# Optimization experiments

Measured on AMD Instinct MI355X. Metric: run time of the kernel, lower is better.

Reference implementation:

```python
import jax, jax.numpy as jnp
import numpy as np

B, N, C = 4, 3136, 64
IMG_H = IMG_W = 56
HEADS = 1
TOPK = 8
HID = 4 * C  # mlp_ratio=4.0


def _ln(x, g, b, eps=1e-5):
    m = x.mean(-1, keepdims=True)
    v = ((x - m) ** 2).mean(-1, keepdims=True)
    return (x - m) * jax.lax.rsqrt(v + eps) * g + b


def _conv(x, w, b, pad, groups):
    y = jax.lax.conv_general_dilated(
        x, w, (1, 1), [(pad, pad), (pad, pad)],
        dimension_numbers=('NCHW', 'OIHW', 'NCHW'), feature_group_count=groups)
    return y + b[None, :, None, None]


def setup_inputs() -> dict:
    key = jax.random.key(0)
    ks = jax.random.split(key, 10)
    def rn(k, shp, scale=0.02):
        return jax.random.normal(k, shp, jnp.float32) * scale
    return {
        'x': jax.random.normal(ks[0], (B, N, C), jnp.float32),
        'norm1_g': jnp.ones((C,), jnp.float32), 'norm1_b': jnp.zeros((C,), jnp.float32),
        'wq': rn(ks[1], (C, C)), 'bq': jnp.zeros((C,), jnp.float32),
        'wkv': rn(ks[2], (C, 2 * C)), 'bkv': jnp.zeros((2 * C,), jnp.float32),
        'wproj': rn(ks[3], (C, C)), 'bproj': jnp.zeros((C,), jnp.float32),
        'local_w': rn(ks[4], (C, C // HEADS, 3, 3), 0.05), 'local_b': jnp.zeros((C,), jnp.float32),
        'norm2_g': jnp.ones((C,), jnp.float32), 'norm2_b': jnp.zeros((C,), jnp.float32),
        'w3': rn(ks[5], (HID, 1, 3, 3), 0.05), 'b3': jnp.zeros((HID,), jnp.float32),
        'w5': rn(ks[6], (HID, 1, 5, 5), 0.05), 'b5': jnp.zeros((HID,), jnp.float32),
        'w1': rn(ks[7], (C, 2 * HID, 1, 1), 0.05), 'b1': jnp.zeros((C,), jnp.float32),
        'H': IMG_H, 'W': IMG_W,
    }


def reference(x, norm1_g, norm1_b, wq, bq, wkv, bkv, wproj, bproj,
              local_w, local_b, norm2_g, norm2_b, w3, b3, w5, b5, w1, b1, H, W):
    Bb, Nn, Cc = x.shape
    d = Cc // HEADS
    scale = d ** -0.5
    # --- DynamicSparseAttention (global branch) ---
    xn = _ln(x, norm1_g, norm1_b)
    q = (xn @ wq + bq).reshape(Bb, Nn, HEADS, d).transpose(0, 2, 1, 3)       # bhnd
    kv = (xn @ wkv + bkv).reshape(Bb, Nn, 2, HEADS, d)
    k = kv[:, :, 0].transpose(0, 2, 1, 3)
    v = kv[:, :, 1].transpose(0, 2, 1, 3)
    attn = jnp.einsum('bhnd,bhmd->bhnm', q, k) * scale                        # [B,h,N,N]
    kth = jax.lax.top_k(attn, TOPK)[0][..., -1:]                              # k-th largest per row
    mask = (attn >= kth).astype(attn.dtype)                                   # top-k scatter mask
    p = jax.nn.softmax(attn * mask, axis=-1)                                  # zeros kept (as in torch ref)
    g = jnp.einsum('bhnm,bhmd->bhnd', p, v).transpose(0, 2, 1, 3).reshape(Bb, Nn, Cc)
    g = g @ wproj + bproj
    # --- local conv attention branch ---
    x_img = x.transpose(0, 2, 1).reshape(Bb, Cc, H, W)
    loc = _conv(x_img, local_w, local_b, 1, HEADS).reshape(Bb, Cc, Nn).transpose(0, 2, 1)
    # --- residual 1 (note: norm1 params reused, as in source) ---
    x = x + _ln(g + loc, norm1_g, norm1_b)
    # --- MSFN ---
    xn2 = _ln(x, norm2_g, norm2_b).transpose(0, 2, 1).reshape(Bb, Cc, H, W)
    x3 = _conv(xn2, w3, b3, 1, Cc)   # depthwise 3x3, channel mult 4
    x5 = _conv(xn2, w5, b5, 2, Cc)   # depthwise 5x5, channel mult 4
    m = _conv(jnp.concatenate([x3, x5], axis=1), w1, b1, 0, 1)
    return x + m.reshape(Bb, Cc, Nn).transpose(0, 2, 1)
```

## Files before the change

### kernel.cpp

```cpp
#include <hip/hip_runtime.h>
#include <math.h>

#define Bv 4
#define Nv 3136
#define Cv 64
#define Hh 56
#define Ww 56
#define HIDv 256
#define TOPKv 8
#define TSP 520
#define LCP 584
#define XNP 72
#define KSPL 8
#define KPS 392

constexpr float SCALE = 0.125f;
constexpr float EPS = 1e-5f;
constexpr float SBIAS = 128.0f;

typedef short bf16x8 __attribute__((ext_vector_type(8)));
typedef float f32x4 __attribute__((ext_vector_type(4)));

#define CSWAP(a, b) { unsigned int _hi = max(a, b); unsigned int _lo = min(a, b); a = _hi; b = _lo; }
#define BITONIC8(T) \
  CSWAP(T[0], T[4]); CSWAP(T[1], T[5]); CSWAP(T[2], T[6]); CSWAP(T[3], T[7]); \
  CSWAP(T[0], T[2]); CSWAP(T[1], T[3]); CSWAP(T[4], T[6]); CSWAP(T[5], T[7]); \
  CSWAP(T[0], T[1]); CSWAP(T[2], T[3]); CSWAP(T[4], T[5]); CSWAP(T[6], T[7]);

__device__ __forceinline__ unsigned short f2bf(float f) {
  unsigned int u = __float_as_uint(f);
  u = (u + 0x7FFFu + ((u >> 16) & 1u)) >> 16;
  return (unsigned short)u;
}
__device__ __forceinline__ float bf2f(unsigned short u) {
  return __uint_as_float(((unsigned int)u) << 16);
}
__device__ __forceinline__ unsigned int pack2(float a, float b) {
  return (unsigned int)f2bf(a) | ((unsigned int)f2bf(b) << 16);
}

__device__ __forceinline__ unsigned int packB(float sb, int j) {
  return (__float_as_uint(sb) & 0xFFFFF000u) | (unsigned int)j;
}

__global__ void k_transpose(const float* __restrict__ w1, const float* __restrict__ lw,
                            const float* __restrict__ w3, const float* __restrict__ w5,
                            const float* __restrict__ wq, const float* __restrict__ wkv,
                            const float* __restrict__ bq, const float* __restrict__ bkv,
                            const float* __restrict__ wproj,
                            unsigned short* __restrict__ w1bf, unsigned short* __restrict__ lwb,
                            float* __restrict__ w3t, float* __restrict__ w5t,
                            unsigned short* __restrict__ wqkvt, float* __restrict__ qkvb,
                            unsigned short* __restrict__ wprojt, float* __restrict__ sumv) {
  int p = blockIdx.x * 256 + threadIdx.x;
  if (p < 256) sumv[p] = 0.0f;
  if (p < 64 * 512) w1bf[p] = f2bf(w1[p]);
  if (p < 64 * 576) {
    int co = p / 576, k = p % 576;
    int tap = k >> 6, ci = k & 63;
    lwb[p] = f2bf(lw[co * 576 + ci * 9 + tap]);
  }
  if (p < 36 * 64) {
    int cin = p & 63, tm = p >> 6;
    int tap = tm >> 2, m = tm & 3;
    w3t[p] = w3[(cin * 4 + m) * 9 + tap];
  }
  if (p < 100 * 64) {
    int cin = p & 63, tm = p >> 6;
    int tap = tm >> 2, m = tm & 3;
    w5t[p] = w5[(cin * 4 + m) * 25 + tap];
  }
  if (p < 192 * 64) {
    int o = p >> 6, i = p & 63;
    float v = (o < 64) ? wq[i * 64 + o] : wkv[i * 128 + (o - 64)];
    wqkvt[p] = f2bf(v);
  }
  if (p < 192) qkvb[p] = (p < 64) ? bq[p] : bkv[p - 64];
  if (p < 64 * 64) {
    int o = p >> 6, i = p & 63;
    wprojt[p] = f2bf(wproj[i * 64 + o]);
  }
}

__global__ __launch_bounds__(256) void k_ln_qkv(
    const float* __restrict__ x, const float* __restrict__ g1, const float* __restrict__ b1,
    const unsigned short* __restrict__ wqkvt, const float* __restrict__ qkvb,
    unsigned short* __restrict__ q16, unsigned short* __restrict__ k16,
    float* __restrict__ vo, float* __restrict__ sumv) {
  __shared__ __align__(16) unsigned short xnS[16 * XNP];
  int bid = blockIdx.x;
  int b = bid / 196, tile = bid % 196;
  size_t tok0 = (size_t)b * Nv + tile * 16;
  int t = threadIdx.x;
  int w = t >> 6, l = t & 63;
  int tokL = t >> 4;
  int ch0 = (t & 15) * 4;
  size_t tok = tok0 + tokL;
  float v[4];
  *(float4*)v = *(const float4*)&x[tok * 64 + ch0];
  float s = v[0] + v[1] + v[2] + v[3];
  float s2 = v[0] * v[0] + v[1] * v[1] + v[2] * v[2] + v[3] * v[3];
#pragma unroll
  for (int off = 1; off <= 8; off <<= 1) {
    s += __shfl_xor(s, off, 64);
    s2 += __shfl_xor(s2, off, 64);
  }
  float m = s * (1.f / 64.f);
  float rs = rsqrtf(s2 * (1.f / 64.f) - m * m + EPS);
  {
    unsigned int pk[2];
    float a0_ = (v[0] - m) * rs * g1[ch0] + b1[ch0];
    float a1_ = (v[1] - m) * rs * g1[ch0 + 1] + b1[ch0 + 1];
    float a2_ = (v[2] - m) * rs * g1[ch0 + 2] + b1[ch0 + 2];
    float a3_ = (v[3] - m) * rs * g1[ch0 + 3] + b1[ch0 + 3];
    pk[0] = pack2(a0_, a1_);
    pk[1] = pack2(a2_, a3_);
    *(uint2*)&xnS[tokL * XNP + ch0] = *(uint2*)pk;
  }
  __syncthreads();
  int n = l & 15, q = l >> 4;
  const bf16x8 a0 = *(const bf16x8*)&xnS[n * XNP + q * 8];
  const bf16x8 a1 = *(const bf16x8*)&xnS[n * XNP + 32 + q * 8];
  {
    const unsigned short* wr = &wqkvt[(size_t)(w * 16 + n) * 64];
    bf16x8 b0 = *(const bf16x8*)&wr[q * 8];
    bf16x8 b1_ = *(const bf16x8*)&wr[32 + q * 8];
    f32x4 acc = {0.f, 0.f, 0.f, 0.f};
    acc = __builtin_amdgcn_mfma_f32_16x16x32_bf16(a0, b0, acc, 0, 0, 0);
    acc = __builtin_amdgcn_mfma_f32_16x16x32_bf16(a1, b1_, acc, 0, 0, 0);
    float bias = qkvb[w * 16 + n];
#pragma unroll
    for (int r = 0; r < 4; ++r)
      q16[(tok0 + q * 4 + r) * 64 + w * 16 + n] = f2bf(acc[r] + bias);
  }
  {
    const unsigned short* wr = &wqkvt[(size_t)((w + 4) * 16 + n) * 64];
    bf16x8 b0 = *(const bf16x8*)&wr[q * 8];
    bf16x8 b1_ = *(const bf16x8*)&wr[32 + q * 8];
    f32x4 acc = {0.f, 0.f, 0.f, 0.f};
    acc = __builtin_amdgcn_mfma_f32_16x16x32_bf16(a0, b0, acc, 0, 0, 0);
    acc = __builtin_amdgcn_mfma_f32_16x16x32_bf16(a1, b1_, acc, 0, 0, 0);
    float bias = qkvb[64 + w * 16 + n];
#pragma unroll
    for (int r = 0; r < 4; ++r)
      k16[(tok0 + q * 4 + r) * 64 + w * 16 + n] = f2bf(acc[r] + bias);
  }
  {
    const unsigned short* wr = &wqkvt[(size_t)((w + 8) * 16 + n) * 64];
    bf16x8 b0 = *(const bf16x8*)&wr[q * 8];
    bf16x8 b1_ = *(const bf16x8*)&wr[32 + q * 8];
    f32x4 acc = {0.f, 0.f, 0.f, 0.f};
    acc = __builtin_amdgcn_mfma_f32_16x16x32_bf16(a0, b0, acc, 0, 0, 0);
    acc = __builtin_amdgcn_mfma_f32_16x16x32_bf16(a1, b1_, acc, 0, 0, 0);
    float bias = qkvb[128 + w * 16 + n];
    float vp = acc[0] + acc[1] + acc[2] + acc[3] + 4.0f * bias;
#pragma unroll
    for (int r = 0; r < 4; ++r)
      vo[(tok0 + q * 4 + r) * 64 + w * 16 + n] = acc[r] + bias;
    vp += __shfl_xor(vp, 16, 64);
    vp += __shfl_xor(vp, 32, 64);
    if (q == 0) atomicAdd(&sumv[b * 64 + w * 16 + n], vp);
  }
}

__global__ __launch_bounds__(128) void k_attn_topk(
    const unsigned short* __restrict__ q16, const unsigned short* __restrict__ k16,
    unsigned int* __restrict__ top8out) {
  int bid = blockIdx.x;
  int w = threadIdx.x >> 6;
  int lane = threadIdx.x & 63;
  int split = ((bid & 3) << 1) | w;
  int lin = bid >> 2;
  int b = lin / 196, tile = lin % 196;
  int qbase = b * Nv + tile * 16;
  size_t bN = (size_t)b * Nv;
  int qcol = lane & 15, quad = lane >> 4;
  int quad4 = quad * 4;

  const bf16x8 qf0 = *(const bf16x8*)&q16[((size_t)(qbase + qcol)) * 64 + quad * 8];
  const bf16x8 qf1 = *(const bf16x8*)&q16[((size_t)(qbase + qcol)) * 64 + 32 + quad * 8];

  unsigned int t8[8];
#pragma unroll
  for (int u = 0; u < 8; ++u) t8[u] = 0u;

  int kbase = split * KPS;
  int m = lane & 15;
  const char* kbp = (const char*)(k16 + bN * 64);
  unsigned int offA = (unsigned int)((kbase + m) * 128 + quad * 16);
  int jbA = kbase + quad4;

  bf16x8 ka0 = *(const bf16x8*)(kbp + offA);
  bf16x8 ka1 = *(const bf16x8*)(kbp + offA + 64);
  bf16x8 kb0 = *(const bf16x8*)(kbp + offA + 2048);
  bf16x8 kb1 = *(const bf16x8*)(kbp + offA + 2112);
  offA += 4096;

#pragma unroll 1
  for (int it = 0; it < 11; ++it) {
    bf16x8 ca0 = ka0, ca1 = ka1, cb0 = kb0, cb1 = kb1;
    ka0 = *(const bf16x8*)(kbp + offA);
    ka1 = *(const bf16x8*)(kbp + offA + 64);
    kb0 = *(const bf16x8*)(kbp + offA + 2048);
    kb1 = *(const bf16x8*)(kbp + offA + 2112);
    offA += 4096;

    f32x4 accA = {SBIAS, SBIAS, SBIAS, SBIAS};
    accA = __builtin_amdgcn_mfma_f32_16x16x32_bf16(ca0, qf0, accA, 0, 0, 0);
    accA = __builtin_amdgcn_mfma_f32_16x16x32_bf16(ca1, qf1, accA, 0, 0, 0);
    f32x4 accB = {SBIAS, SBIAS, SBIAS, SBIAS};
    accB = __builtin_amdgcn_mfma_f32_16x16x32_bf16(cb0, qf0, accB, 0, 0, 0);
    accB = __builtin_amdgcn_mfma_f32_16x16x32_bf16(cb1, qf1, accB, 0, 0, 0);

    unsigned int p0 = packB(accA[0], jbA + 0);
    unsigned int p1 = packB(accA[1], jbA + 1);
    unsigned int p2 = packB(accA[2], jbA + 2);
    unsigned int p3 = packB(accA[3], jbA + 3);
    unsigned int q0 = packB(accB[0], jbA + 16);
    unsigned int q1 = packB(accB[1], jbA + 17);
    unsigned int q2 = packB(accB[2], jbA + 18);
    unsigned int q3 = packB(accB[3], jbA + 19);
    jbA += 32;
    CSWAP(p0, p1); CSWAP(p2, p3); CSWAP(p0, p2); CSWAP(p1, p3); CSWAP(p1, p2);
    CSWAP(q0, q1); CSWAP(q2, q3); CSWAP(q0, q2); CSWAP(q1, q3); CSWAP(q1, q2);
    unsigned int u8[8] = {p0, p1, p2, p3, q3, q2, q1, q0};
    BITONIC8(u8);
    t8[0] = max(t8[0], u8[7]);
    t8[1] = max(t8[1], u8[6]);
    t8[2] = max(t8[2], u8[5]);
    t8[3] = max(t8[3], u8[4]);
    t8[4] = max(t8[4], u8[3]);
    t8[5] = max(t8[5], u8[2]);
    t8[6] = max(t8[6], u8[1]);
    t8[7] = max(t8[7], u8[0]);
    BITONIC8(t8);
  }

  {
    bf16x8 ca0 = ka0, ca1 = ka1, cb0 = kb0, cb1 = kb1;
    ka0 = *(const bf16x8*)(kbp + offA);
    ka1 = *(const bf16x8*)(kbp + offA + 64);

    f32x4 accA = {SBIAS, SBIAS, SBIAS, SBIAS};
    accA = __builtin_amdgcn_mfma_f32_16x16x32_bf16(ca0, qf0, accA, 0, 0, 0);
    accA = __builtin_amdgcn_mfma_f32_16x16x32_bf16(ca1, qf1, accA, 0, 0, 0);
    f32x4 accB = {SBIAS, SBIAS, SBIAS, SBIAS};
    accB = __builtin_amdgcn_mfma_f32_16x16x32_bf16(cb0, qf0, accB, 0, 0, 0);
    accB = __builtin_amdgcn_mfma_f32_16x16x32_bf16(cb1, qf1, accB, 0, 0, 0);

    unsigned int p0 = packB(accA[0], jbA + 0);
    unsigned int p1 = packB(accA[1], jbA + 1);
    unsigned int p2 = packB(accA[2], jbA + 2);
    unsigned int p3 = packB(accA[3], jbA + 3);
    unsigned int q0 = packB(accB[0], jbA + 16);
    unsigned int q1 = packB(accB[1], jbA + 17);
    unsigned int q2 = packB(accB[2], jbA + 18);
    unsigned int q3 = packB(accB[3], jbA + 19);
    jbA += 32;
    CSWAP(p0, p1); CSWAP(p2, p3); CSWAP(p0, p2); CSWAP(p1, p3); CSWAP(p1, p2);
    CSWAP(q0, q1); CSWAP(q2, q3); CSWAP(q0, q2); CSWAP(q1, q3); CSWAP(q1, q2);
    unsigned int u8[8] = {p0, p1, p2, p3, q3, q2, q1, q0};
    BITONIC8(u8);
    t8[0] = max(t8[0], u8[7]);
    t8[1] = max(t8[1], u8[6]);
    t8[2] = max(t8[2], u8[5]);
    t8[3] = max(t8[3], u8[4]);
    t8[4] = max(t8[4], u8[3]);
    t8[5] = max(t8[5], u8[2]);
    t8[6] = max(t8[6], u8[1]);
    t8[7] = max(t8[7], u8[0]);
    BITONIC8(t8);
  }

  {
    f32x4 accA = {SBIAS, SBIAS, SBIAS, SBIAS};
    accA = __builtin_amdgcn_mfma_f32_16x16x32_bf16(ka0, qf0, accA, 0, 0, 0);
    accA = __builtin_amdgcn_mfma_f32_16x16x32_bf16(ka1, qf1, accA, 0, 0, 0);
    bool val = quad < 2;
    unsigned int p0 = val ? packB(accA[0], jbA + 0) : 0u;
    unsigned int p1 = val ? packB(accA[1], jbA + 1) : 0u;
    unsigned int p2 = val ? packB(accA[2], jbA + 2) : 0u;
    unsigned int p3 = val ? packB(accA[3], jbA + 3) : 0u;
    CSWAP(p0, p1); CSWAP(p2, p3); CSWAP(p0, p2); CSWAP(p1, p3); CSWAP(p1, p2);
    t8[4] = max(t8[4], p3);
    t8[5] = max(t8[5], p2);
    t8[6] = max(t8[6], p1);
    t8[7] = max(t8[7], p0);
    BITONIC8(t8);
  }

#pragma unroll
  for (int step = 16; step <= 32; step <<= 1) {
    unsigned int o[8];
#pragma unroll
    for (int i = 0; i < 8; ++i) o[i] = (unsigned int)__shfl_xor((int)t8[i], step, 64);
    unsigned int nw[8];
#pragma unroll
    for (int i = 0; i < 8; ++i) nw[i] = max(t8[i], o[7 - i]);
#pragma unroll
    for (int i = 0; i < 8; ++i) t8[i] = nw[i];
    BITONIC8(t8);
  }
  if (quad == 0) {
    size_t obase = ((size_t)(bN + tile * 16 + qcol)) * 64 + split * 8;
    *(uint4*)&top8out[obase] = make_uint4(t8[0], t8[1], t8[2], t8[3]);
    *(uint4*)&top8out[obase + 4] = make_uint4(t8[4], t8[5], t8[6], t8[7]);
  }
}

__global__ __launch_bounds__(256) void k_attn_proj(
    const unsigned int* __restrict__ top8, const float* __restrict__ vg,
    const float* __restrict__ sumv, const float* __restrict__ x,
    const unsigned short* __restrict__ lwb, const float* __restrict__ lb,
    const unsigned short* __restrict__ wprojt, const float* __restrict__ bproj,
    const float* __restrict__ g1, const float* __restrict__ b1,
    const float* __restrict__ g2, const float* __restrict__ b2,
    float* __restrict__ x2, unsigned short* __restrict__ xn2b) {
  __shared__ float kwS[16][8];
  __shared__ int kidxS[16][8];
  __shared__ float invZS[16];
  __shared__ __align__(16) unsigned short imS[16 * LCP];
  __shared__ __align__(16) unsigned short gS[16 * XNP];
  __shared__ float yS[16 * 66];
  int bid = blockIdx.x;
  int b = bid / 196, rem = bid % 196;
  int th = rem / 7, tw = rem % 7;
  int h0 = th * 2, w0 = tw * 8;
  size_t bN = (size_t)b * Nv;
  int t = threadIdx.x;

  for (int p = t; p < 1152; p += 256) {
    int sub = p & 7, s = p >> 3;
    int tok = s / 9, tap = s % 9;
    int tr = tok >> 3, tc = tok & 7;
    int dh = tap / 3, dw = tap % 3;
    int gh = h0 + tr - 1 + dh, gw = w0 + tc - 1 + dw;
    uint4 uu = {0u, 0u, 0u, 0u};
    if (gh >= 0 && gh < Hh && gw >= 0 && gw < Ww) {
      const float* xp = &x[(bN + gh * Ww + gw) * 64 + sub * 8];
      float4 va = *(const float4*)xp;
      float4 vb = *(const float4*)(xp + 4);
      uu.x = pack2(va.x, va.y);
      uu.y = pack2(va.z, va.w);
      uu.z = pack2(vb.x, vb.y);
      uu.w = pack2(vb.z, vb.w);
    }
    *(uint4*)&imS[tok * LCP + tap * 64 + sub * 8] = uu;
  }

  if (t < 16) {
    int gtok = (h0 + (t >> 3)) * Ww + w0 + (t & 7);
    size_t base = (bN + gtok) * 64;
    unsigned int A[8];
#pragma unroll
    for (int i = 0; i < 8; ++i) A[i] = top8[base + i];
#pragma unroll
    for (int h = 1; h < 8; ++h) {
      unsigned int Bb[8];
#pragma unroll
      for (int i = 0; i < 8; ++i) Bb[i] = top8[base + h * 8 + i];
#pragma unroll
      for (int i = 0; i < 8; ++i) A[i] = max(A[i], Bb[7 - i]);
      BITONIC8(A);
    }
    float Z = (float)(Nv - TOPKv);
#pragma unroll
    for (int u = 0; u < 8; ++u) {
      float sb = __uint_as_float(A[u] & 0xFFFFF000u);
      float s = (sb - SBIAS) * SCALE;
      float e = __expf(s);
      kwS[t][u] = e - 1.0f;
      kidxS[t][u] = (int)(A[u] & 0xFFFu);
      Z += e;
    }
    invZS[t] = 1.0f / Z;
  }
  __syncthreads();

  int w = t >> 6, l = t & 63;
  int n = l & 15, q = l >> 4;

  f32x4 lacc = {0.f, 0.f, 0.f, 0.f};
  {
    const unsigned short* lwrow = &lwb[(size_t)(w * 16 + n) * 576];
#pragma unroll 6
    for (int kk = 0; kk < 18; ++kk) {
      bf16x8 af = *(const bf16x8*)&imS[n * LCP + kk * 32 + q * 8];
      bf16x8 bfr = *(const bf16x8*)&lwrow[kk * 32 + q * 8];
      lacc = __builtin_amdgcn_mfma_f32_16x16x32_bf16(af, bfr, lacc, 0, 0, 0);
    }
  }
  float lbias = lb[w * 16 + n];

  {
    int c = t & 63, rg = t >> 6;
    float sv = sumv[b * 64 + c];
#pragma unroll
    for (int rr = 0; rr < 4; ++rr) {
      int tokL = rg * 4 + rr;
      float acc = sv;
#pragma unroll
      for (int u = 0; u < 8; ++u)
        acc += kwS[tokL][u] * vg[(bN + kidxS[tokL][u]) * 64 + c];
      gS[tokL * XNP + c] = f2bf(acc * invZS[tokL]);
    }
  }
  __syncthreads();

  {
    const bf16x8 a0 = *(const bf16x8*)&gS[n * XNP + q * 8];
    const bf16x8 a1 = *(const bf16x8*)&gS[n * XNP + 32 + q * 8];
    const unsigned short* wr = &wprojt[(size_t)(w * 16 + n) * 64];
    bf16x8 b0 = *(const bf16x8*)&wr[q * 8];
    bf16x8 b1_ = *(const bf16x8*)&wr[32 + q * 8];
    f32x4 acc = {0.f, 0.f, 0.f, 0.f};
    acc = __builtin_amdgcn_mfma_f32_16x16x32_bf16(a0, b0, acc, 0, 0, 0);
    acc = __builtin_amdgcn_mfma_f32_16x16x32_bf16(a1, b1_, acc, 0, 0, 0);
    float bias = bproj[w * 16 + n];
#pragma unroll
    for (int r = 0; r < 4; ++r)
      yS[(q * 4 + r) * 66 + w * 16 + n] = acc[r] + bias + lacc[r] + lbias;
  }
  __syncthreads();

  int tokL = t >> 4;
  int ch0 = (t & 15) * 4;
  size_t tok = bN + (size_t)(h0 + (tokL >> 3)) * Ww + w0 + (tokL & 7);
  float y[4];
#pragma unroll
  for (int i = 0; i < 4; ++i) y[i] = yS[tokL * 66 + ch0 + i];
  float s = y[0] + y[1] + y[2] + y[3];
  float s2 = y[0] * y[0] + y[1] * y[1] + y[2] * y[2] + y[3] * y[3];
#pragma unroll
  for (int off = 1; off <= 8; off <<= 1) {
    s += __shfl_xor(s, off, 64);
    s2 += __shfl_xor(s2, off, 64);
  }
  float m1 = s * (1.f / 64.f);
  float rs1 = rsqrtf(s2 * (1.f / 64.f) - m1 * m1 + EPS);
  float xv[4];
  *(float4*)xv = *(const float4*)&x[tok * 64 + ch0];
  float x2v[4];
  float t_s = 0.f, t_s2 = 0.f;
#pragma unroll
  for (int i = 0; i < 4; ++i) {
    float t1 = (y[i] - m1) * rs1 * g1[ch0 + i] + b1[ch0 + i];
    x2v[i] = xv[i] + t1;
    t_s += x2v[i];
    t_s2 += x2v[i] * x2v[i];
  }
#pragma unroll
  for (int off = 1; off <= 8; off <<= 1) {
    t_s += __shfl_xor(t_s, off, 64);
    t_s2 += __shfl_xor(t_s2, off, 64);
  }
  float m2 = t_s * (1.f / 64.f);
  float rs2 = rsqrtf(t_s2 * (1.f / 64.f) - m2 * m2 + EPS);
  *(float4*)&x2[tok * 64 + ch0] = *(float4*)x2v;
  unsigned int pk[2];
  {
    float a0_ = (x2v[0] - m2) * rs2 * g2[ch0] + b2[ch0];
    float a1_ = (x2v[1] - m2) * rs2 * g2[ch0 + 1] + b2[ch0 + 1];
    float a2_ = (x2v[2] - m2) * rs2 * g2[ch0 + 2] + b2[ch0 + 2];
    float a3_ = (x2v[3] - m2) * rs2 * g2[ch0 + 3] + b2[ch0 + 3];
    pk[0] = pack2(a0_, a1_);
    pk[1] = pack2(a2_, a3_);
  }
  *(uint2*)&xn2b[tok * 64 + ch0] = *(uint2*)pk;
}

__global__ __launch_bounds__(256) void k_msfn(
    const unsigned short* __restrict__ xn2b, const float* __restrict__ x2,
    const float* __restrict__ w3t, const float* __restrict__ b3,
    const float* __restrict__ w5t, const float* __restrict__ b5,
    const unsigned short* __restrict__ w1bf, const float* __restrict__ b1,
    float* __restrict__ out) {
  __shared__ __align__(16) unsigned short xtS[6 * 12 * 64];
  __shared__ __align__(16) unsigned short tsS[16 * TSP];

  int bid = blockIdx.x;
  int b = bid / 196;
  int rem = bid % 196;
  int th = rem / 7, tw = rem % 7;
  int h0 = th * 2, w0 = tw * 8;
  size_t bN = (size_t)b * Nv;
  int t = threadIdx.x;

  unsigned int* xtU = (unsigned int*)xtS;
  for (int p = t; p < 6 * 12 * 32; p += 256) {
    int cp = p & 31, rc = p >> 5;
    int r = rc / 12, cc = rc % 12;
    int gh = h0 - 2 + r, gw = w0 - 2 + cc;
    unsigned int v = 0;
    if (gh >= 0 && gh < Hh && gw >= 0 && gw < Ww)
      v = *(const unsigned int*)&xn2b[(bN + gh * Ww + gw) * 64 + cp * 2];
    xtU[rc * 32 + cp] = v;
  }
  __syncthreads();

  int cin = t & 63, tg = t >> 6;
  int tr = tg >> 1, tc0 = (tg & 1) * 4;
  float win[5][8];
#pragma unroll
  for (int r = 0; r < 5; ++r)
#pragma unroll
    for (int c = 0; c < 8; ++c)
      win[r][c] = bf2f(xtS[((tr + r) * 12 + tc0 + c) * 64 + cin]);

  unsigned int* tsU = (unsigned int*)tsS;
#pragma unroll 1
  for (int m2 = 0; m2 < 4; m2 += 2) {
    float a3[2][9], a5[2][25], bb3[2], bb5[2];
#pragma unroll
    for (int mm = 0; mm < 2; ++mm) {
      int m = m2 + mm;
#pragma unroll
      for (int tap = 0; tap < 9; ++tap) a3[mm][tap] = w3t[(tap * 4 + m) * 64 + cin];
#pragma unroll
      for (int tap = 0; tap < 25; ++tap) a5[mm][tap] = w5t[(tap * 4 + m) * 64 + cin];
      bb3[mm] = b3[cin * 4 + m];
      bb5[mm] = b5[cin * 4 + m];
    }
#pragma unroll
    for (int tk = 0; tk < 4; ++tk) {
      int tok = tg * 4 + tk;
      unsigned int p3 = 0, p5 = 0;
#pragma unroll
      for (int mm = 0; mm < 2; ++mm) {
        float acc3 = bb3[mm];
#pragma unroll
        for (int kh = 0; kh < 3; ++kh)
#pragma unroll
          for (int kw2 = 0; kw2 < 3; ++kw2)
            acc3 += win[1 + kh][tk + 1 + kw2] * a3[mm][kh * 3 + kw2];
        float acc5 = bb5[mm];
#pragma unroll
        for (int kh = 0; kh < 5; ++kh)
#pragma unroll
          for (int kw2 = 0; kw2 < 5; ++kw2)
            acc5 += win[kh][tk + kw2] * a5[mm][kh * 5 + kw2];
        p3 |= (unsigned int)f2bf(acc3) << (16 * mm);
        p5 |= (unsigned int)f2bf(acc5) << (16 * mm);
      }
      tsU[(tok * TSP + cin * 4 + m2) >> 1] = p3;
      tsU[(tok * TSP + 256 + cin * 4 + m2) >> 1] = p5;
    }
  }
  __syncthreads();

  int wv = tg, lane = t & 63;
  int n16 = lane & 15, quad = lane >> 4;
  const unsigned short* wrow = &w1bf[(size_t)(wv * 16 + n16) * 512];
  f32x4 acc = {0.f, 0.f, 0.f, 0.f};
#pragma unroll 4
  for (int kk = 0; kk < 16; ++kk) {
    bf16x8 af = *(const bf16x8*)&tsS[n16 * TSP + kk * 32 + quad * 8];
    bf16x8 bfr = *(const bf16x8*)&wrow[kk * 32 + quad * 8];
    acc = __builtin_amdgcn_mfma_f32_16x16x32_bf16(af, bfr, acc, 0, 0, 0);
  }
  float bias = b1[wv * 16 + n16];
#pragma unroll
  for (int r = 0; r < 4; ++r) {
    int tok = quad * 4 + r;
    int trr = tok >> 3, tcc = tok & 7;
    size_t idx = (bN + (size_t)(h0 + trr) * Ww + w0 + tcc) * 64 + wv * 16 + n16;
    out[idx] = x2[idx] + acc[r] + bias;
  }
}

extern "C" void kernel_launch(void* const* d_in, const int* in_sizes, int n_in,
                              void* d_out, int out_size, void* d_ws, size_t ws_size,
                              hipStream_t stream) {
  const float* x = (const float*)d_in[0];
  const float* n1g = (const float*)d_in[1];
  const float* n1b = (const float*)d_in[2];
  const float* wq = (const float*)d_in[3];
  const float* bq = (const float*)d_in[4];
  const float* wkv = (const float*)d_in[5];
  const float* bkv = (const float*)d_in[6];
  const float* wproj = (const float*)d_in[7];
  const float* bproj = (const float*)d_in[8];
  const float* lw = (const float*)d_in[9];
  const float* lb = (const float*)d_in[10];
  const float* n2g = (const float*)d_in[11];
  const float* n2b = (const float*)d_in[12];
  const float* w3 = (const float*)d_in[13];
  const float* b3 = (const float*)d_in[14];
  const float* w5 = (const float*)d_in[15];
  const float* b5 = (const float*)d_in[16];
  const float* w1 = (const float*)d_in[17];
  const float* b1 = (const float*)d_in[18];
  float* out = (float*)d_out;

  float* ws = (float*)d_ws;
  const size_t TOK = (size_t)Bv * Nv * Cv;
  float* vb = ws;
  float* sumv = vb + TOK;
  float* x2 = sumv + 256;
  float* w3t = x2 + TOK;
  float* w5t = w3t + 2304;
  float* qkvb = w5t + 6400;
  unsigned short* q16 = (unsigned short*)(qkvb + 192);
  unsigned short* k16 = q16 + TOK;
  unsigned short* xn2b = k16 + TOK;
  unsigned short* w1bf = xn2b + TOK;
  unsigned short* lwb = w1bf + 64 * 512;
  unsigned short* wqkvt = lwb + 64 * 576;
  unsigned short* wprojt = wqkvt + 192 * 64;
  unsigned int* top8ws = (unsigned int*)(wprojt + 64 * 64 + 64);

  k_transpose<<<144, 256, 0, stream>>>(w1, lw, w3, w5, wq, wkv, bq, bkv, wproj,
                                       w1bf, lwb, w3t, w5t, wqkvt, qkvb, wprojt, sumv);
  k_ln_qkv<<<Bv * 196, 256, 0, stream>>>(x, n1g, n1b, wqkvt, qkvb, q16, k16, vb, sumv);
  k_attn_topk<<<Bv * 196 * 4, 128, 0, stream>>>(q16, k16, top8ws);
  k_attn_proj<<<Bv * 196, 256, 0, stream>>>(top8ws, vb, sumv, x, lwb, lb, wprojt, bproj,
                                            n1g, n1b, n2g, n2b, x2, xn2b);
  k_msfn<<<Bv * 196, 256, 0, stream>>>(xn2b, x2, w3t, b3, w5t, b5, w1bf, b1, out);
}
```

Baseline: 188.1 us.

## Reuse key fragments across four query tiles in the top-k attention kernel

Each wave in the score/top-k kernel now handles 64 queries (four 16-query MFMA tiles) against one key chunk, so every loaded key fragment feeds four query tiles instead of one. To keep enough blocks in flight, keys are split 16 ways of 196 each instead of 8 ways of 392. The per-split top-8 buffer therefore doubles to 16 partial lists per token, and the downstream projection kernel merges 16 lists instead of 8. This trades more registers per thread (four running top-8 lists, with a 3-blocks-per-CU launch bound) and more merge work for less key-load traffic.

```diff
diff --git a/kernel.cpp b/kernel.cpp
--- a/kernel.cpp
+++ b/kernel.cpp
@@ -11,8 +11,8 @@
 #define TSP 520
 #define LCP 584
 #define XNP 72
-#define KSPL 8
-#define KPS 392
+#define KSPL 16
+#define KPS 196
 
 constexpr float SCALE = 0.125f;
 constexpr float EPS = 1e-5f;
@@ -163,26 +163,55 @@
   }
 }
 
-__global__ __launch_bounds__(128) void k_attn_topk(
+#define PAIRMERGE(T, accA, accB, jb) { \
+    unsigned int _p0 = packB(accA[0], (jb) + 0); \
+    unsigned int _p1 = packB(accA[1], (jb) + 1); \
+    unsigned int _p2 = packB(accA[2], (jb) + 2); \
+    unsigned int _p3 = packB(accA[3], (jb) + 3); \
+    unsigned int _q0 = packB(accB[0], (jb) + 16); \
+    unsigned int _q1 = packB(accB[1], (jb) + 17); \
+    unsigned int _q2 = packB(accB[2], (jb) + 18); \
+    unsigned int _q3 = packB(accB[3], (jb) + 19); \
+    CSWAP(_p0, _p1); CSWAP(_p2, _p3); CSWAP(_p0, _p2); CSWAP(_p1, _p3); CSWAP(_p1, _p2); \
+    CSWAP(_q0, _q1); CSWAP(_q2, _q3); CSWAP(_q0, _q2); CSWAP(_q1, _q3); CSWAP(_q1, _q2); \
+    unsigned int _u8[8] = {_p0, _p1, _p2, _p3, _q3, _q2, _q1, _q0}; \
+    BITONIC8(_u8); \
+    T[0] = max(T[0], _u8[7]); \
+    T[1] = max(T[1], _u8[6]); \
+    T[2] = max(T[2], _u8[5]); \
+    T[3] = max(T[3], _u8[4]); \
+    T[4] = max(T[4], _u8[3]); \
+    T[5] = max(T[5], _u8[2]); \
+    T[6] = max(T[6], _u8[1]); \
+    T[7] = max(T[7], _u8[0]); \
+    BITONIC8(T); }
+
+__global__ __launch_bounds__(128, 3) void k_attn_topk(
     const unsigned short* __restrict__ q16, const unsigned short* __restrict__ k16,
     unsigned int* __restrict__ top8out) {
   int bid = blockIdx.x;
   int w = threadIdx.x >> 6;
   int lane = threadIdx.x & 63;
-  int split = ((bid & 3) << 1) | w;
-  int lin = bid >> 2;
-  int b = lin / 196, tile = lin % 196;
-  int qbase = b * Nv + tile * 16;
+  int split = ((bid & 7) << 1) | w;
+  int lin = bid >> 3;
+  int b = lin / 49, tg = lin % 49;
+  int qbase = b * Nv + tg * 64;
   size_t bN = (size_t)b * Nv;
   int qcol = lane & 15, quad = lane >> 4;
   int quad4 = quad * 4;
 
-  const bf16x8 qf0 = *(const bf16x8*)&q16[((size_t)(qbase + qcol)) * 64 + quad * 8];
-  const bf16x8 qf1 = *(const bf16x8*)&q16[((size_t)(qbase + qcol)) * 64 + 32 + quad * 8];
-
-  unsigned int t8[8];
-#pragma unroll
-  for (int u = 0; u < 8; ++u) t8[u] = 0u;
+  bf16x8 qf0a[4], qf1a[4];
+#pragma unroll
+  for (int tt = 0; tt < 4; ++tt) {
+    qf0a[tt] = *(const bf16x8*)&q16[((size_t)(qbase + tt * 16 + qcol)) * 64 + quad * 8];
+    qf1a[tt] = *(const bf16x8*)&q16[((size_t)(qbase + tt * 16 + qcol)) * 64 + 32 + quad * 8];
+  }
+
+  unsigned int t8[4][8];
+#pragma unroll
+  for (int tt = 0; tt < 4; ++tt)
+#pragma unroll
+    for (int u = 0; u < 8; ++u) t8[tt][u] = 0u;
 
   int kbase = split * KPS;
   int m = lane & 15;
@@ -197,7 +226,7 @@
   offA += 4096;
 
 #pragma unroll 1
-  for (int it = 0; it < 11; ++it) {
+  for (int it = 0; it < 5; ++it) {
     bf16x8 ca0 = ka0, ca1 = ka1, cb0 = kb0, cb1 = kb1;
     ka0 = *(const bf16x8*)(kbp + offA);
     ka1 = *(const bf16x8*)(kbp + offA + 64);
@@ -205,35 +234,17 @@
     kb1 = *(const bf16x8*)(kbp + offA + 2112);
     offA += 4096;
 
-    f32x4 accA = {SBIAS, SBIAS, SBIAS, SBIAS};
-    accA = __builtin_amdgcn_mfma_f32_16x16x32_bf16(ca0, qf0, accA, 0, 0, 0);
-    accA = __builtin_amdgcn_mfma_f32_16x16x32_bf16(ca1, qf1, accA, 0, 0, 0);
-    f32x4 accB = {SBIAS, SBIAS, SBIAS, SBIAS};
-    accB = __builtin_amdgcn_mfma_f32_16x16x32_bf16(cb0, qf0, accB, 0, 0, 0);
-    accB = __builtin_amdgcn_mfma_f32_16x16x32_bf16(cb1, qf1, accB, 0, 0, 0);
-
-    unsigned int p0 = packB(accA[0], jbA + 0);
-    unsigned int p1 = packB(accA[1], jbA + 1);
-    unsigned int p2 = packB(accA[2], jbA + 2);
-    unsigned int p3 = packB(accA[3], jbA + 3);
-    unsigned int q0 = packB(accB[0], jbA + 16);
-    unsigned int q1 = packB(accB[1], jbA + 17);
-    unsigned int q2 = packB(accB[2], jbA + 18);
-    unsigned int q3 = packB(accB[3], jbA + 19);
+#pragma unroll
+    for (int tt = 0; tt < 4; ++tt) {
+      f32x4 accA = {SBIAS, SBIAS, SBIAS, SBIAS};
+      accA = __builtin_amdgcn_mfma_f32_16x16x32_bf16(ca0, qf0a[tt], accA, 0, 0, 0);
+      accA = __builtin_amdgcn_mfma_f32_16x16x32_bf16(ca1, qf1a[tt], accA, 0, 0, 0);
+      f32x4 accB = {SBIAS, SBIAS, SBIAS, SBIAS};
+      accB = __builtin_amdgcn_mfma_f32_16x16x32_bf16(cb0, qf0a[tt], accB, 0, 0, 0);
+      accB = __builtin_amdgcn_mfma_f32_16x16x32_bf16(cb1, qf1a[tt], accB, 0, 0, 0);
+      PAIRMERGE(t8[tt], accA, accB, jbA);
+    }
     jbA += 32;
-    CSWAP(p0, p1); CSWAP(p2, p3); CSWAP(p0, p2); CSWAP(p1, p3); CSWAP(p1, p2);
-    CSWAP(q0, q1); CSWAP(q2, q3); CSWAP(q0, q2); CSWAP(q1, q3); CSWAP(q1, q2);
-    unsigned int u8[8] = {p0, p1, p2, p3, q3, q2, q1, q0};
-    BITONIC8(u8);
-    t8[0] = max(t8[0], u8[7]);
-    t8[1] = max(t8[1], u8[6]);
-    t8[2] = max(t8[2], u8[5]);
-    t8[3] = max(t8[3], u8[4]);
-    t8[4] = max(t8[4], u8[3]);
-    t8[5] = max(t8[5], u8[2]);
-    t8[6] = max(t8[6], u8[1]);
-    t8[7] = max(t8[7], u8[0]);
-    BITONIC8(t8);
   }
 
   {
@@ -241,70 +252,58 @@
     ka0 = *(const bf16x8*)(kbp + offA);
     ka1 = *(const bf16x8*)(kbp + offA + 64);
 
-    f32x4 accA = {SBIAS, SBIAS, SBIAS, SBIAS};
-    accA = __builtin_amdgcn_mfma_f32_16x16x32_bf16(ca0, qf0, accA, 0, 0, 0);
-    accA = __builtin_amdgcn_mfma_f32_16x16x32_bf16(ca1, qf1, accA, 0, 0, 0);
-    f32x4 accB = {SBIAS, SBIAS, SBIAS, SBIAS};
-    accB = __builtin_amdgcn_mfma_f32_16x16x32_bf16(cb0, qf0, accB, 0, 0, 0);
-    accB = __builtin_amdgcn_mfma_f32_16x16x32_bf16(cb1, qf1, accB, 0, 0, 0);
-
-    unsigned int p0 = packB(accA[0], jbA + 0);
-    unsigned int p1 = packB(accA[1], jbA + 1);
-    unsigned int p2 = packB(accA[2], jbA + 2);
-    unsigned int p3 = packB(accA[3], jbA + 3);
-    unsigned int q0 = packB(accB[0], jbA + 16);
-    unsigned int q1 = packB(accB[1], jbA + 17);
-    unsigned int q2 = packB(accB[2], jbA + 18);
-    unsigned int q3 = packB(accB[3], jbA + 19);
+#pragma unroll
+    for (int tt = 0; tt < 4; ++tt) {
+      f32x4 accA = {SBIAS, SBIAS, SBIAS, SBIAS};
+      accA = __builtin_amdgcn_mfma_f32_16x16x32_bf16(ca0, qf0a[tt], accA, 0, 0, 0);
+      accA = __builtin_amdgcn_mfma_f32_16x16x32_bf16(ca1, qf1a[tt], accA, 0, 0, 0);
+      f32x4 accB = {SBIAS, SBIAS, SBIAS, SBIAS};
+      accB = __builtin_amdgcn_mfma_f32_16x16x32_bf16(cb0, qf0a[tt], accB, 0, 0, 0);
+      accB = __builtin_amdgcn_mfma_f32_16x16x32_bf16(cb1, qf1a[tt], accB, 0, 0, 0);
+      PAIRMERGE(t8[tt], accA, accB, jbA);
+    }
     jbA += 32;
-    CSWAP(p0, p1); CSWAP(p2, p3); CSWAP(p0, p2); CSWAP(p1, p3); CSWAP(p1, p2);
-    CSWAP(q0, q1); CSWAP(q2, q3); CSWAP(q0, q2); CSWAP(q1, q3); CSWAP(q1, q2);
-    unsigned int u8[8] = {p0, p1, p2, p3, q3, q2, q1, q0};
-    BITONIC8(u8);
-    t8[0] = max(t8[0], u8[7]);
-    t8[1] = max(t8[1], u8[6]);
-    t8[2] = max(t8[2], u8[5]);
-    t8[3] = max(t8[3], u8[4]);
-    t8[4] = max(t8[4], u8[3]);
-    t8[5] = max(t8[5], u8[2]);
-    t8[6] = max(t8[6], u8[1]);
-    t8[7] = max(t8[7], u8[0]);
-    BITONIC8(t8);
-  }
-
-  {
-    f32x4 accA = {SBIAS, SBIAS, SBIAS, SBIAS};
-    accA = __builtin_amdgcn_mfma_f32_16x16x32_bf16(ka0, qf0, accA, 0, 0, 0);
-    accA = __builtin_amdgcn_mfma_f32_16x16x32_bf16(ka1, qf1, accA, 0, 0, 0);
-    bool val = quad < 2;
-    unsigned int p0 = val ? packB(accA[0], jbA + 0) : 0u;
-    unsigned int p1 = val ? packB(accA[1], jbA + 1) : 0u;
-    unsigned int p2 = val ? packB(accA[2], jbA + 2) : 0u;
-    unsigned int p3 = val ? packB(accA[3], jbA + 3) : 0u;
-    CSWAP(p0, p1); CSWAP(p2, p3); CSWAP(p0, p2); CSWAP(p1, p3); CSWAP(p1, p2);
-    t8[4] = max(t8[4], p3);
-    t8[5] = max(t8[5], p2);
-    t8[6] = max(t8[6], p1);
-    t8[7] = max(t8[7], p0);
-    BITONIC8(t8);
-  }
-
-#pragma unroll
-  for (int step = 16; step <= 32; step <<= 1) {
-    unsigned int o[8];
-#pragma unroll
-    for (int i = 0; i < 8; ++i) o[i] = (unsigned int)__shfl_xor((int)t8[i], step, 64);
-    unsigned int nw[8];
-#pragma unroll
-    for (int i = 0; i < 8; ++i) nw[i] = max(t8[i], o[7 - i]);
-#pragma unroll
-    for (int i = 0; i < 8; ++i) t8[i] = nw[i];
-    BITONIC8(t8);
-  }
-  if (quad == 0) {
-    size_t obase = ((size_t)(bN + tile * 16 + qcol)) * 64 + split * 8;
-    *(uint4*)&top8out[obase] = make_uint4(t8[0], t8[1], t8[2], t8[3]);
-    *(uint4*)&top8out[obase + 4] = make_uint4(t8[4], t8[5], t8[6], t8[7]);
+  }
+
+  {
+    bool val = quad == 0;
+#pragma unroll
+    for (int tt = 0; tt < 4; ++tt) {
+      f32x4 accA = {SBIAS, SBIAS, SBIAS, SBIAS};
+      accA = __builtin_amdgcn_mfma_f32_16x16x32_bf16(ka0, qf0a[tt], accA, 0, 0, 0);
+      accA = __builtin_amdgcn_mfma_f32_16x16x32_bf16(ka1, qf1a[tt], accA, 0, 0, 0);
+      unsigned int p0 = val ? packB(accA[0], jbA + 0) : 0u;
+      unsigned int p1 = val ? packB(accA[1], jbA + 1) : 0u;
+      unsigned int p2 = val ? packB(accA[2], jbA + 2) : 0u;
+      unsigned int p3 = val ? packB(accA[3], jbA + 3) : 0u;
+      CSWAP(p0, p1); CSWAP(p2, p3); CSWAP(p0, p2); CSWAP(p1, p3); CSWAP(p1, p2);
+      t8[tt][4] = max(t8[tt][4], p3);
+      t8[tt][5] = max(t8[tt][5], p2);
+      t8[tt][6] = max(t8[tt][6], p1);
+      t8[tt][7] = max(t8[tt][7], p0);
+      BITONIC8(t8[tt]);
+    }
+  }
+
+#pragma unroll
+  for (int tt = 0; tt < 4; ++tt) {
+#pragma unroll
+    for (int step = 16; step <= 32; step <<= 1) {
+      unsigned int o[8];
+#pragma unroll
+      for (int i = 0; i < 8; ++i) o[i] = (unsigned int)__shfl_xor((int)t8[tt][i], step, 64);
+      unsigned int nw[8];
+#pragma unroll
+      for (int i = 0; i < 8; ++i) nw[i] = max(t8[tt][i], o[7 - i]);
+#pragma unroll
+      for (int i = 0; i < 8; ++i) t8[tt][i] = nw[i];
+      BITONIC8(t8[tt]);
+    }
+    if (quad == 0) {
+      size_t obase = ((size_t)(bN + tg * 64 + tt * 16 + qcol)) * 128 + split * 8;
+      *(uint4*)&top8out[obase] = make_uint4(t8[tt][0], t8[tt][1], t8[tt][2], t8[tt][3]);
+      *(uint4*)&top8out[obase + 4] = make_uint4(t8[tt][4], t8[tt][5], t8[tt][6], t8[tt][7]);
+    }
   }
 }
 
@@ -350,12 +349,12 @@
 
   if (t < 16) {
     int gtok = (h0 + (t >> 3)) * Ww + w0 + (t & 7);
-    size_t base = (bN + gtok) * 64;
+    size_t base = (bN + gtok) * 128;
     unsigned int A[8];
 #pragma unroll
     for (int i = 0; i < 8; ++i) A[i] = top8[base + i];
 #pragma unroll
-    for (int h = 1; h < 8; ++h) {
+    for (int h = 1; h < 16; ++h) {
       unsigned int Bb[8];
 #pragma unroll
       for (int i = 0; i < 8; ++i) Bb[i] = top8[base + h * 8 + i];
@@ -612,7 +611,7 @@
   k_transpose<<<144, 256, 0, stream>>>(w1, lw, w3, w5, wq, wkv, bq, bkv, wproj,
                                        w1bf, lwb, w3t, w5t, wqkvt, qkvb, wprojt, sumv);
   k_ln_qkv<<<Bv * 196, 256, 0, stream>>>(x, n1g, n1b, wqkvt, qkvb, q16, k16, vb, sumv);
-  k_attn_topk<<<Bv * 196 * 4, 128, 0, stream>>>(q16, k16, top8ws);
+  k_attn_topk<<<Bv * 49 * 8, 128, 0, stream>>>(q16, k16, top8ws);
   k_attn_proj<<<Bv * 196, 256, 0, stream>>>(top8ws, vb, sumv, x, lwb, lb, wprojt, bproj,
                                             n1g, n1b, n2g, n2b, x2, xn2b);
   k_msfn<<<Bv * 196, 256, 0, stream>>>(xn2b, x2, w3t, b3, w5t, b5, w1bf, b1, out);
```

Result: faster. 172.1 us (-8.5%).
